# Kernel tuning notes

Hardware: AMD Instinct MI355X
Metric: run time of the kernel (lower is better)

## Reference

```python
import jax, jax.numpy as jnp
import numpy as np

L = 4        # initial_layers (layers actually run in forward)
DIM = 128    # model dim
NB = 8       # num_blocks per layer
K = 2        # max_active blocks per layer
B = 131072   # batch
FIN = 32     # input features (nn.Linear(32, dim))
PRIORITY = 0.5  # fresh block: success_rate*0.6 + excitement*0.4 = 0.5


def setup_inputs() -> dict:
    key = jax.random.key(0)
    ks = jax.random.split(key, 10)
    s = 0.02
    return {
        "x": jax.random.normal(ks[0], (B, FIN), dtype=jnp.float32),
        "proj_w": jax.random.normal(ks[1], (FIN, DIM)) * s,
        "proj_b": jnp.zeros((DIM,)),
        "pos": jax.random.normal(ks[2], (1, 16, DIM)) * 0.02,
        "sel_w": jax.random.normal(ks[3], (L, DIM, NB)) * s,   # per-layer selector
        "sel_b": jnp.zeros((L, NB)),
        "ln_s": jnp.ones((L, NB, DIM)),                         # per-block LayerNorm
        "ln_b": jnp.zeros((L, NB, DIM)),
        "w1": jax.random.normal(ks[4], (L, NB, DIM, 2 * DIM)) * s,
        "b1": jnp.zeros((L, NB, 2 * DIM)),
        "w2": jax.random.normal(ks[5], (L, NB, 2 * DIM, DIM)) * s,
        "b2": jnp.zeros((L, NB, DIM)),
        "gate": jax.random.normal(ks[6], (L, NB, DIM)) * 0.01,  # torsion_gate
        "cls_w": jax.random.normal(ks[7], (DIM, 2)) * s,
        "cls_b": jnp.zeros((2,)),
        "torsion_field": jnp.zeros((1, DIM)),                   # registered buffer (zeros)
    }


def _block(h, ln_s, ln_b, w1, b1, w2, b2, gate, tf):
    # h: [B, 1, DIM]. LayerNorm(eps=1e-5) -> Linear -> GELU -> Linear -> torsion gate -> 0.5 residual
    mu = h.mean(axis=-1, keepdims=True)
    var = ((h - mu) ** 2).mean(axis=-1, keepdims=True)
    hn = (h - mu) / jnp.sqrt(var + 1e-5) * ln_s + ln_b
    z = jax.nn.gelu(hn @ w1 + b1, approximate=False) @ w2 + b2
    te = jax.nn.sigmoid(gate) * tf           # [1, DIM]
    z = z * (1.0 + te[:, None, :])           # broadcast over seq dim (unsqueeze(1))
    return h + 0.5 * z


def reference(x, proj_w, proj_b, pos, sel_w, sel_b, ln_s, ln_b,
              w1, b1, w2, b2, gate, cls_w, cls_b, torsion_field):
    # input projection + positional slice; seq_len == 1
    h = (x @ proj_w + proj_b)[:, None, :] + pos[:, :1, :]   # [B, 1, DIM]
    for l in range(L):
        scores = jax.nn.sigmoid(h.mean(axis=1) @ sel_w[l] + sel_b[l])  # [B, NB]
        # adjusted[0, i] = scores[0, i]*0.6 + priority*0.4 ; top-k taken on row 0
        adj = scores[0] * 0.6 + PRIORITY * 0.4
        _, top = jax.lax.top_k(adj, K)
        for k in range(K):
            i = top[k]
            h = _block(h, ln_s[l][i], ln_b[l][i], w1[l][i], b1[l][i],
                       w2[l][i], b2[l][i], gate[l][i], torsion_field)
    logits = h.mean(axis=1) @ cls_w + cls_b   # [B, 2]
    return logits, h
```

## Files before the change

### kernel.cpp

```cpp
#include <hip/hip_runtime.h>


typedef __attribute__((ext_vector_type(8))) short s16x8;
typedef __attribute__((ext_vector_type(4))) float f32x4;
typedef unsigned short ushort_t;

#define BATCH 131072
#define TBROWS 64
#define HSTR 132
#define FGSTR 544
#define FQSTR 136

#define WS_IDX 0
#define WS_PRM 64
#define WS_PB  12352
#define WS_PW  12864
#define WS_W1  21056
#define WS_W2  545344
#define WS_DMP 1069632

__device__ inline ushort_t f2bf(float f) {
  unsigned u = __float_as_uint(f);
  u += 0x7fffu + ((u >> 16) & 1u);
  return (ushort_t)(u >> 16);
}
__device__ inline ushort_t f2bf1(float f) {
  return (ushort_t)((__float_as_uint(f) + 0x8000u) >> 16);
}
__device__ inline unsigned f2bf2(float lo, float hi) {
  unsigned a = __float_as_uint(lo) + 0x8000u;
  unsigned b = __float_as_uint(hi) + 0x8000u;
  return __builtin_amdgcn_perm(b, a, 0x07060302u);
}

__device__ inline float geluf(float v) {
  float e = __builtin_amdgcn_exp2f(-2.4554670f * v);
  return v * __builtin_amdgcn_rcpf(1.0f + e);
}

__global__ __launch_bounds__(256) void uv6_warm(
    const float* __restrict__ w1, const float* __restrict__ w2,
    float* __restrict__ dump) {
  int gid = blockIdx.x * 256 + threadIdx.x;
  const float4* a = (const float4*)w1;
  const float4* b = (const float4*)w2;
  float s = 0.0f;
#pragma unroll
  for (int i = 0; i < 2; ++i) {
    float4 v = a[gid + i * 131072];
    float4 u = b[gid + i * 131072];
    s += v.x + v.y + v.z + v.w + u.x + u.y + u.z + u.w;
  }
  if (s > 1e30f) dump[0] = s;
}

__global__ __launch_bounds__(1024) void uv6_select(
    const float* __restrict__ x, const float* __restrict__ proj_w,
    const float* __restrict__ proj_b, const float* __restrict__ pos,
    const float* __restrict__ sel_w, const float* __restrict__ sel_b,
    const float* __restrict__ ln_s, const float* __restrict__ ln_b,
    const float* __restrict__ w1, const float* __restrict__ b1,
    const float* __restrict__ w2, const float* __restrict__ b2,
    const float* __restrict__ gate, const float* __restrict__ tf,
    int* __restrict__ wsI) {
  __shared__ float h0[128], hn[128], z1[256];
  __shared__ float red[1024];
  __shared__ float wred[128];
  __shared__ float adjs[8];
  __shared__ int top[2];
  __shared__ float stat[2];
  const int t = threadIdx.x;
  const int lane = t & 63, wv = t >> 6;
  const int n1 = t & 255, dp1 = t >> 8;
  const int n2 = t & 127, dp2 = t >> 7;

  if (t < 128) {
    float a = proj_b[t] + pos[t];
#pragma unroll
    for (int f = 0; f < 32; ++f) a += x[f] * proj_w[f * 128 + t];
    h0[t] = a;
  }
  __syncthreads();

  for (int l = 0; l < 4; ++l) {
    {
      float pp = h0[t >> 3] * sel_w[(l * 128 + (t >> 3)) * 8 + (t & 7)];
      pp += __shfl_xor(pp, 8);
      pp += __shfl_xor(pp, 16);
      pp += __shfl_xor(pp, 32);
      if (lane < 8) wred[wv * 8 + lane] = pp;
    }
    __syncthreads();
    if (t < 8) {
      float sc = sel_b[l * 8 + t];
#pragma unroll
      for (int v = 0; v < 16; ++v) sc += wred[v * 8 + t];
      sc = 1.0f / (1.0f + __expf(-sc));
      adjs[t] = sc * 0.6f + 0.2f;
    }
    __syncthreads();
    if (t == 0) {
      int i0 = 0; float v0 = adjs[0];
      for (int j = 1; j < 8; ++j) if (adjs[j] > v0) { v0 = adjs[j]; i0 = j; }
      int i1 = -1; float v1 = -1e30f;
      for (int j = 0; j < 8; ++j) if (j != i0 && adjs[j] > v1) { v1 = adjs[j]; i1 = j; }
      top[0] = i0; top[1] = i1;
      wsI[2 * l] = i0; wsI[2 * l + 1] = i1;
    }
    __syncthreads();
    for (int kk = 0; kk < 2; ++kk) {
      const int base = l * 8 + top[kk];
      float w1v[32], w2v[32];
      const float* w1p = w1 + (base * 128 + dp1 * 32) * 256 + n1;
      const float* w2p = w2 + (base * 256 + dp2 * 32) * 128 + n2;
#pragma unroll
      for (int j = 0; j < 32; ++j) w1v[j] = w1p[j * 256];
#pragma unroll
      for (int j = 0; j < 32; ++j) w2v[j] = w2p[j * 128];
      if (t < 64) {
        float a = h0[t], b = h0[t + 64];
        float s2 = a + b, q2 = a * a + b * b;
        s2 += __shfl_xor(s2, 1);  q2 += __shfl_xor(q2, 1);
        s2 += __shfl_xor(s2, 2);  q2 += __shfl_xor(q2, 2);
        s2 += __shfl_xor(s2, 4);  q2 += __shfl_xor(q2, 4);
        s2 += __shfl_xor(s2, 8);  q2 += __shfl_xor(q2, 8);
        s2 += __shfl_xor(s2, 16); q2 += __shfl_xor(q2, 16);
        s2 += __shfl_xor(s2, 32); q2 += __shfl_xor(q2, 32);
        if (t == 0) {
          float mu = s2 * (1.0f / 128.0f);
          stat[0] = mu;
          stat[1] = rsqrtf(q2 * (1.0f / 128.0f) - mu * mu + 1e-5f);
        }
      }
      __syncthreads();
      if (t < 128)
        hn[t] = (h0[t] - stat[0]) * stat[1] * ln_s[base * 128 + t] + ln_b[base * 128 + t];
      __syncthreads();
      {
        float a = 0.0f;
#pragma unroll
        for (int j = 0; j < 32; ++j) a += hn[dp1 * 32 + j] * w1v[j];
        red[dp1 * 256 + n1] = a;
      }
      __syncthreads();
      if (t < 256) {
        float z = red[t] + red[256 + t] + red[512 + t] + red[768 + t] + b1[base * 256 + t];
        z1[t] = z * 0.5f * (1.0f + erff(z * 0.70710678118f));
      }
      __syncthreads();
      {
        float a = 0.0f;
#pragma unroll
        for (int j = 0; j < 32; ++j) a += z1[dp2 * 32 + j] * w2v[j];
        red[dp2 * 128 + n2] = a;
      }
      __syncthreads();
      if (t < 128) {
        float z2 = b2[base * 128 + t];
#pragma unroll
        for (int v = 0; v < 8; ++v) z2 += red[v * 128 + t];
        float te = tf[t] * (1.0f / (1.0f + __expf(-gate[base * 128 + t])));
        h0[t] += 0.5f * z2 * (1.0f + te);
      }
      __syncthreads();
    }
  }
}

__global__ __launch_bounds__(256) void uv6_pack(
    const float* __restrict__ w1, const float* __restrict__ w2,
    const float* __restrict__ ln_s, const float* __restrict__ ln_b,
    const float* __restrict__ b1, const float* __restrict__ b2,
    const float* __restrict__ gate, const float* __restrict__ tf,
    const float* __restrict__ proj_w, const float* __restrict__ proj_b,
    const float* __restrict__ pos, const int* __restrict__ wsI,
    ushort_t* __restrict__ w1P, ushort_t* __restrict__ w2P,
    float* __restrict__ wsP, ushort_t* __restrict__ pwP,
    float* __restrict__ pb) {
  const int bx = blockIdx.x;
  if (bx < 2048) {
    int gid = bx * 256 + threadIdx.x;
    int s = gid >> 16, e = gid & 65535;
    int base = (s >> 1) * 8 + wsI[s];
    if (e < 32768) {
      int j = e & 7, ln = (e >> 3) & 63, ks = (e >> 9) & 3, nt = e >> 11;
      int k = ks * 32 + (ln >> 4) * 8 + j;
      int n = nt * 16 + (ln & 15);
      w1P[s * 32768 + e] = f2bf(w1[(base * 128 + k) * 256 + n] * ln_s[base * 128 + k]);
    } else {
      int e2 = e - 32768;
      int j = e2 & 7, ln = (e2 >> 3) & 63, ks = (e2 >> 9) & 7, nt = e2 >> 12;
      int k = ks * 32 + (ln >> 4) * 8 + j;
      int n = nt * 16 + (ln & 15);
      float te = tf[n] * (1.0f / (1.0f + __expf(-gate[base * 128 + n])));
      w2P[s * 32768 + e2] = f2bf(w2[(base * 256 + k) * 128 + n] * (0.5f * (1.0f + te)));
    }
    return;
  }
  if (bx < 2056) {
    int s = bx - 2048, n = threadIdx.x;
    int base = (s >> 1) * 8 + wsI[s];
    float a = b1[base * 256 + n];
#pragma unroll 16
    for (int k = 0; k < 128; ++k)
      a += ln_b[base * 128 + k] * w1[(base * 128 + k) * 256 + n];
    wsP[s * 384 + n] = a;
    if (n < 128) {
      float te = tf[n] * (1.0f / (1.0f + __expf(-gate[base * 128 + n])));
      wsP[s * 384 + 256 + n] = 0.5f * (1.0f + te) * b2[base * 128 + n];
    }
    return;
  }
  int gid = (bx - 2056) * 256 + threadIdx.x;
  if (gid < 4096) {
    int j = gid & 7, ln = (gid >> 3) & 63, nt = gid >> 9;
    int k = (ln >> 4) * 8 + j, n = nt * 16 + (ln & 15);
    pwP[gid] = f2bf(proj_w[k * 128 + n]);
  } else if (gid < 4224) {
    int d = gid - 4096;
    pb[d] = proj_b[d] + pos[d];
  }
}

__global__ __launch_bounds__(512, 2) void uv6_main(
    const float* __restrict__ x, const float* __restrict__ cls_w,
    const float* __restrict__ cls_b, const float* __restrict__ wsP,
    const float* __restrict__ pb, const ushort_t* __restrict__ pwP,
    const ushort_t* __restrict__ w1P, const ushort_t* __restrict__ w2P,
    float* __restrict__ out) {
  __shared__ float hbuf[TBROWS * HSTR];
  __shared__ ushort_t frag[32 * FGSTR];

  const int tid = threadIdx.x;
  const int w = tid >> 6, lane = tid & 63, q = lane >> 4, m0 = lane & 15;
  const int r = tid >> 3, p = tid & 7;
  const int rt_r = r >> 4, m_r = r & 15;
  const long rowbase = (long)blockIdx.x * TBROWS;

  {
    float4 xv = *(const float4*)(x + (rowbase + r) * 32 + p * 4);
    unsigned u01 = f2bf2(xv.x, xv.y), u23 = f2bf2(xv.z, xv.w);
    ushort_t* dst = &frag[(rt_r * 8) * FGSTR + (p >> 1) * FQSTR + m_r * 8 + (p & 1) * 4];
    *(unsigned*)dst = u01;
    *(unsigned*)(dst + 2) = u23;
  }
  __syncthreads();

  {
    s16x8 bfr = *(const s16x8*)(pwP + (w * 64 + lane) * 8);
    float bv = pb[w * 16 + m0];
    f32x4 acc[4];
#pragma unroll
    for (int rt = 0; rt < 4; ++rt) acc[rt] = (f32x4){bv, bv, bv, bv};
#pragma unroll
    for (int rt = 0; rt < 4; ++rt) {
      s16x8 af = *(const s16x8*)&frag[(rt * 8) * FGSTR + q * FQSTR + m0 * 8];
      acc[rt] = __builtin_amdgcn_mfma_f32_16x16x32_bf16(af, bfr, acc[rt], 0, 0, 0);
    }
    int col = w * 16 + m0;
#pragma unroll
    for (int rt = 0; rt < 4; ++rt)
#pragma unroll
      for (int reg = 0; reg < 4; ++reg)
        hbuf[(rt * 16 + 4 * q + reg) * HSTR + col] = acc[rt][reg];
  }
  __syncthreads();

  float* outH = out + (size_t)BATCH * 2;

  for (int s = 0; s < 8; ++s) {
    const float* c1 = wsP + s * 384;
    const float* c2 = c1 + 256;
    const ushort_t* w1s = w1P + s * 32768;
    const ushort_t* w2s = w2P + s * 32768;

    s16x8 bfr1[2][4];
#pragma unroll
    for (int ni = 0; ni < 2; ++ni)
#pragma unroll
      for (int ks = 0; ks < 4; ++ks)
        bfr1[ni][ks] = *(const s16x8*)(w1s + (((2 * w + ni) * 4 + ks) * 64 + lane) * 8);

    {
      const float* hr = hbuf + r * HSTR + p * 16;
      float hv[16];
      *(float4*)(hv) = *(const float4*)(hr);
      *(float4*)(hv + 4) = *(const float4*)(hr + 4);
      *(float4*)(hv + 8) = *(const float4*)(hr + 8);
      *(float4*)(hv + 12) = *(const float4*)(hr + 12);
      float sum = 0.0f, ssq = 0.0f;
#pragma unroll
      for (int i = 0; i < 16; ++i) { sum += hv[i]; ssq += hv[i] * hv[i]; }
      sum += __shfl_xor(sum, 1); ssq += __shfl_xor(ssq, 1);
      sum += __shfl_xor(sum, 2); ssq += __shfl_xor(ssq, 2);
      sum += __shfl_xor(sum, 4); ssq += __shfl_xor(ssq, 4);
      float mu = sum * (1.0f / 128.0f);
      float rstd = rsqrtf(ssq * (1.0f / 128.0f) - mu * mu + 1e-5f);
      float nmu = -mu * rstd;
#pragma unroll
      for (int g = 0; g < 2; ++g) {
        union { unsigned u[4]; s16x8 v; } tv;
#pragma unroll
        for (int jj = 0; jj < 4; ++jj) {
          float a = fmaf(hv[g * 8 + jj * 2], rstd, nmu);
          float b = fmaf(hv[g * 8 + jj * 2 + 1], rstd, nmu);
          tv.u[jj] = f2bf2(a, b);
        }
        int kb = p >> 1, qq = (2 * p + g) & 3;
        *(s16x8*)&frag[(rt_r * 8 + kb) * FGSTR + qq * FQSTR + m_r * 8] = tv.v;
      }
    }
    __syncthreads();

    f32x4 a1[4][2];
    {
#pragma unroll
      for (int ni = 0; ni < 2; ++ni) {
        float bv = c1[(2 * w + ni) * 16 + m0];
#pragma unroll
        for (int rt = 0; rt < 4; ++rt) a1[rt][ni] = (f32x4){bv, bv, bv, bv};
      }
#pragma unroll
      for (int ks = 0; ks < 4; ++ks) {
        s16x8 af[4];
#pragma unroll
        for (int rt = 0; rt < 4; ++rt)
          af[rt] = *(const s16x8*)&frag[(rt * 8 + ks) * FGSTR + q * FQSTR + m0 * 8];
#pragma unroll
        for (int rt = 0; rt < 4; ++rt)
#pragma unroll
          for (int ni = 0; ni < 2; ++ni)
            a1[rt][ni] = __builtin_amdgcn_mfma_f32_16x16x32_bf16(af[rt], bfr1[ni][ks], a1[rt][ni], 0, 0, 0);
      }
    }
    __syncthreads();

    s16x8 bfr2[8];
#pragma unroll
    for (int ks = 0; ks < 8; ++ks)
      bfr2[ks] = *(const s16x8*)(w2s + ((w * 8 + ks) * 64 + lane) * 8);
    f32x4 a2[4];
    {
      float bv = c2[w * 16 + m0];
#pragma unroll
      for (int rt = 0; rt < 4; ++rt) a2[rt] = (f32x4){bv, bv, bv, bv};
    }

    {
      int j = m0 & 7;
#pragma unroll
      for (int ni = 0; ni < 2; ++ni) {
        int qq = (2 * ni + (m0 >> 3)) & 3;
#pragma unroll
        for (int rt = 0; rt < 4; ++rt)
#pragma unroll
          for (int reg = 0; reg < 4; ++reg)
            frag[(rt * 8 + w) * FGSTR + qq * FQSTR + (4 * q + reg) * 8 + j] =
                f2bf1(geluf(a1[rt][ni][reg]));
      }
    }
    __syncthreads();

    {
#pragma unroll
      for (int kb = 0; kb < 8; ++kb) {
        s16x8 af[4];
#pragma unroll
        for (int rt = 0; rt < 4; ++rt)
          af[rt] = *(const s16x8*)&frag[(rt * 8 + kb) * FGSTR + q * FQSTR + m0 * 8];
#pragma unroll
        for (int rt = 0; rt < 4; ++rt)
          a2[rt] = __builtin_amdgcn_mfma_f32_16x16x32_bf16(af[rt], bfr2[kb], a2[rt], 0, 0, 0);
      }
    }

    {
      int col = w * 16 + m0;
#pragma unroll
      for (int rt = 0; rt < 4; ++rt)
#pragma unroll
        for (int reg = 0; reg < 4; ++reg)
          hbuf[(rt * 16 + 4 * q + reg) * HSTR + col] += a2[rt][reg];
    }
    __syncthreads();
  }

#pragma unroll
  for (int it = 0; it < 4; ++it) {
    int p4 = it * 512 + tid;
    int row = p4 >> 5, c = (p4 & 31) * 4;
    float4 o = *(const float4*)(hbuf + row * HSTR + c);
    *(float4*)(outH + rowbase * 128 + p4 * 4) = o;
  }

  {
    const float* hr = hbuf + r * HSTR + p * 16;
    float l0 = 0.0f, l1 = 0.0f;
#pragma unroll
    for (int i = 0; i < 16; i += 4) {
      float4 v = *(const float4*)(hr + i);
      int c = (p * 16 + i) * 2;
      l0 += v.x * cls_w[c] + v.y * cls_w[c + 2] + v.z * cls_w[c + 4] + v.w * cls_w[c + 6];
      l1 += v.x * cls_w[c + 1] + v.y * cls_w[c + 3] + v.z * cls_w[c + 5] + v.w * cls_w[c + 7];
    }
    l0 += __shfl_xor(l0, 1); l1 += __shfl_xor(l1, 1);
    l0 += __shfl_xor(l0, 2); l1 += __shfl_xor(l1, 2);
    l0 += __shfl_xor(l0, 4); l1 += __shfl_xor(l1, 4);
    if (p == 0) {
      float2 lg = {l0 + cls_b[0], l1 + cls_b[1]};
      *(float2*)(out + (rowbase + r) * 2) = lg;
    }
  }
}

extern "C" void kernel_launch(void* const* d_in, const int* in_sizes, int n_in,
                              void* d_out, int out_size, void* d_ws, size_t ws_size,
                              hipStream_t stream) {
  (void)in_sizes; (void)n_in; (void)out_size; (void)ws_size;
  const float* x      = (const float*)d_in[0];
  const float* proj_w = (const float*)d_in[1];
  const float* proj_b = (const float*)d_in[2];
  const float* pos    = (const float*)d_in[3];
  const float* sel_w  = (const float*)d_in[4];
  const float* sel_b  = (const float*)d_in[5];
  const float* ln_s   = (const float*)d_in[6];
  const float* ln_b   = (const float*)d_in[7];
  const float* w1     = (const float*)d_in[8];
  const float* b1     = (const float*)d_in[9];
  const float* w2     = (const float*)d_in[10];
  const float* b2     = (const float*)d_in[11];
  const float* gate   = (const float*)d_in[12];
  const float* cls_w  = (const float*)d_in[13];
  const float* cls_b  = (const float*)d_in[14];
  const float* tf     = (const float*)d_in[15];

  char* ws = (char*)d_ws;
  int* wsI        = (int*)(ws + WS_IDX);
  float* wsP      = (float*)(ws + WS_PRM);
  float* pb       = (float*)(ws + WS_PB);
  ushort_t* pwP   = (ushort_t*)(ws + WS_PW);
  ushort_t* w1P   = (ushort_t*)(ws + WS_W1);
  ushort_t* w2P   = (ushort_t*)(ws + WS_W2);
  float* dump     = (float*)(ws + WS_DMP);
  float* outF     = (float*)d_out;

  uv6_warm<<<512, 256, 0, stream>>>(w1, w2, dump);
  uv6_select<<<1, 1024, 0, stream>>>(x, proj_w, proj_b, pos, sel_w, sel_b, ln_s,
                                     ln_b, w1, b1, w2, b2, gate, tf, wsI);
  uv6_pack<<<2073, 256, 0, stream>>>(w1, w2, ln_s, ln_b, b1, b2, gate, tf,
                                     proj_w, proj_b, pos, wsI, w1P, w2P, wsP,
                                     pwP, pb);
  uv6_main<<<BATCH / TBROWS, 512, 0, stream>>>(x, cls_w, cls_b, wsP, pb, pwP,
                                               w1P, w2P, outF);
}
```

Baseline: 363.3 us.

## Halve main kernel block to 256 threads with doubled per-wave tiles and DPP reductions

The main fused MLP kernel now runs 4 waves per 64-row tile instead of 8. Each wave computes twice as many output columns in every GEMM stage (projection, W1 and W2), and each thread handles 32 columns for LayerNorm and the classifier. The cross-lane reductions switch from shfl_xor to DPP quad permutes. The aim is to reuse each A fragment read from LDS across more MFMAs, cut barrier participants and shuffle cost, at the expense of many more registers per thread (16 W1 fragments, 16 W2 fragments and 16 accumulators), which can cut occupancy or spill.

```diff
diff --git a/kernel.cpp b/kernel.cpp
--- a/kernel.cpp
+++ b/kernel.cpp
@@ -31,6 +31,15 @@
   unsigned a = __float_as_uint(lo) + 0x8000u;
   unsigned b = __float_as_uint(hi) + 0x8000u;
   return __builtin_amdgcn_perm(b, a, 0x07060302u);
+}
+
+__device__ inline float dpp_xor1(float v) {
+  return __int_as_float(__builtin_amdgcn_update_dpp(
+      0, __float_as_int(v), 0xB1 , 0xF, 0xF, true));
+}
+__device__ inline float dpp_xor2(float v) {
+  return __int_as_float(__builtin_amdgcn_update_dpp(
+      0, __float_as_int(v), 0x4E , 0xF, 0xF, true));
 }
 
 __device__ inline float geluf(float v) {
@@ -222,7 +231,7 @@
   }
 }
 
-__global__ __launch_bounds__(512, 2) void uv6_main(
+__global__ __launch_bounds__(256, 2) void uv6_main(
     const float* __restrict__ x, const float* __restrict__ cls_w,
     const float* __restrict__ cls_b, const float* __restrict__ wsP,
     const float* __restrict__ pb, const ushort_t* __restrict__ pwP,
@@ -233,36 +242,46 @@
 
   const int tid = threadIdx.x;
   const int w = tid >> 6, lane = tid & 63, q = lane >> 4, m0 = lane & 15;
-  const int r = tid >> 3, p = tid & 7;
+  const int r = tid >> 2, p = tid & 3;
   const int rt_r = r >> 4, m_r = r & 15;
   const long rowbase = (long)blockIdx.x * TBROWS;
 
   {
-    float4 xv = *(const float4*)(x + (rowbase + r) * 32 + p * 4);
-    unsigned u01 = f2bf2(xv.x, xv.y), u23 = f2bf2(xv.z, xv.w);
-    ushort_t* dst = &frag[(rt_r * 8) * FGSTR + (p >> 1) * FQSTR + m_r * 8 + (p & 1) * 4];
-    *(unsigned*)dst = u01;
-    *(unsigned*)(dst + 2) = u23;
+    const float4* xp = (const float4*)(x + (rowbase + r) * 32 + p * 8);
+    float4 x0 = xp[0], x1 = xp[1];
+    union { unsigned u[4]; s16x8 v; } tv;
+    tv.u[0] = f2bf2(x0.x, x0.y); tv.u[1] = f2bf2(x0.z, x0.w);
+    tv.u[2] = f2bf2(x1.x, x1.y); tv.u[3] = f2bf2(x1.z, x1.w);
+    *(s16x8*)&frag[(rt_r * 8) * FGSTR + p * FQSTR + m_r * 8] = tv.v;
   }
   __syncthreads();
 
   {
-    s16x8 bfr = *(const s16x8*)(pwP + (w * 64 + lane) * 8);
-    float bv = pb[w * 16 + m0];
-    f32x4 acc[4];
-#pragma unroll
-    for (int rt = 0; rt < 4; ++rt) acc[rt] = (f32x4){bv, bv, bv, bv};
+    s16x8 bp0 = *(const s16x8*)(pwP + ((2 * w + 0) * 64 + lane) * 8);
+    s16x8 bp1 = *(const s16x8*)(pwP + ((2 * w + 1) * 64 + lane) * 8);
+    float bv0 = pb[(2 * w + 0) * 16 + m0];
+    float bv1 = pb[(2 * w + 1) * 16 + m0];
+    f32x4 acc[4][2];
+#pragma unroll
+    for (int rt = 0; rt < 4; ++rt) {
+      acc[rt][0] = (f32x4){bv0, bv0, bv0, bv0};
+      acc[rt][1] = (f32x4){bv1, bv1, bv1, bv1};
+    }
 #pragma unroll
     for (int rt = 0; rt < 4; ++rt) {
       s16x8 af = *(const s16x8*)&frag[(rt * 8) * FGSTR + q * FQSTR + m0 * 8];
-      acc[rt] = __builtin_amdgcn_mfma_f32_16x16x32_bf16(af, bfr, acc[rt], 0, 0, 0);
-    }
-    int col = w * 16 + m0;
+      acc[rt][0] = __builtin_amdgcn_mfma_f32_16x16x32_bf16(af, bp0, acc[rt][0], 0, 0, 0);
+      acc[rt][1] = __builtin_amdgcn_mfma_f32_16x16x32_bf16(af, bp1, acc[rt][1], 0, 0, 0);
+    }
 #pragma unroll
     for (int rt = 0; rt < 4; ++rt)
 #pragma unroll
-      for (int reg = 0; reg < 4; ++reg)
-        hbuf[(rt * 16 + 4 * q + reg) * HSTR + col] = acc[rt][reg];
+      for (int ni = 0; ni < 2; ++ni) {
+        int col = (2 * w + ni) * 16 + m0;
+#pragma unroll
+        for (int reg = 0; reg < 4; ++reg)
+          hbuf[(rt * 16 + 4 * q + reg) * HSTR + col] = acc[rt][ni][reg];
+      }
   }
   __syncthreads();
 
@@ -274,138 +293,138 @@
     const ushort_t* w1s = w1P + s * 32768;
     const ushort_t* w2s = w2P + s * 32768;
 
-    s16x8 bfr1[2][4];
-#pragma unroll
-    for (int ni = 0; ni < 2; ++ni)
+    s16x8 bfr1[4][4];
+#pragma unroll
+    for (int ni = 0; ni < 4; ++ni)
 #pragma unroll
       for (int ks = 0; ks < 4; ++ks)
-        bfr1[ni][ks] = *(const s16x8*)(w1s + (((2 * w + ni) * 4 + ks) * 64 + lane) * 8);
+        bfr1[ni][ks] = *(const s16x8*)(w1s + (((4 * w + ni) * 4 + ks) * 64 + lane) * 8);
 
     {
-      const float* hr = hbuf + r * HSTR + p * 16;
-      float hv[16];
-      *(float4*)(hv) = *(const float4*)(hr);
-      *(float4*)(hv + 4) = *(const float4*)(hr + 4);
-      *(float4*)(hv + 8) = *(const float4*)(hr + 8);
-      *(float4*)(hv + 12) = *(const float4*)(hr + 12);
+      const float* hr = hbuf + r * HSTR + p * 32;
+      float hv[32];
+#pragma unroll
+      for (int i = 0; i < 8; ++i)
+        *(float4*)(hv + i * 4) = *(const float4*)(hr + i * 4);
       float sum = 0.0f, ssq = 0.0f;
 #pragma unroll
-      for (int i = 0; i < 16; ++i) { sum += hv[i]; ssq += hv[i] * hv[i]; }
-      sum += __shfl_xor(sum, 1); ssq += __shfl_xor(ssq, 1);
-      sum += __shfl_xor(sum, 2); ssq += __shfl_xor(ssq, 2);
-      sum += __shfl_xor(sum, 4); ssq += __shfl_xor(ssq, 4);
+      for (int i = 0; i < 32; ++i) { sum += hv[i]; ssq += hv[i] * hv[i]; }
+      sum += dpp_xor1(sum); ssq += dpp_xor1(ssq);
+      sum += dpp_xor2(sum); ssq += dpp_xor2(ssq);
       float mu = sum * (1.0f / 128.0f);
       float rstd = rsqrtf(ssq * (1.0f / 128.0f) - mu * mu + 1e-5f);
       float nmu = -mu * rstd;
 #pragma unroll
-      for (int g = 0; g < 2; ++g) {
+      for (int kq = 0; kq < 4; ++kq) {
         union { unsigned u[4]; s16x8 v; } tv;
 #pragma unroll
         for (int jj = 0; jj < 4; ++jj) {
-          float a = fmaf(hv[g * 8 + jj * 2], rstd, nmu);
-          float b = fmaf(hv[g * 8 + jj * 2 + 1], rstd, nmu);
+          float a = fmaf(hv[kq * 8 + jj * 2], rstd, nmu);
+          float b = fmaf(hv[kq * 8 + jj * 2 + 1], rstd, nmu);
           tv.u[jj] = f2bf2(a, b);
         }
-        int kb = p >> 1, qq = (2 * p + g) & 3;
-        *(s16x8*)&frag[(rt_r * 8 + kb) * FGSTR + qq * FQSTR + m_r * 8] = tv.v;
-      }
-    }
-    __syncthreads();
-
-    f32x4 a1[4][2];
-    {
-#pragma unroll
-      for (int ni = 0; ni < 2; ++ni) {
-        float bv = c1[(2 * w + ni) * 16 + m0];
-#pragma unroll
-        for (int rt = 0; rt < 4; ++rt) a1[rt][ni] = (f32x4){bv, bv, bv, bv};
-      }
-#pragma unroll
-      for (int ks = 0; ks < 4; ++ks) {
-        s16x8 af[4];
-#pragma unroll
-        for (int rt = 0; rt < 4; ++rt)
-          af[rt] = *(const s16x8*)&frag[(rt * 8 + ks) * FGSTR + q * FQSTR + m0 * 8];
-#pragma unroll
-        for (int rt = 0; rt < 4; ++rt)
-#pragma unroll
-          for (int ni = 0; ni < 2; ++ni)
-            a1[rt][ni] = __builtin_amdgcn_mfma_f32_16x16x32_bf16(af[rt], bfr1[ni][ks], a1[rt][ni], 0, 0, 0);
-      }
-    }
-    __syncthreads();
-
-    s16x8 bfr2[8];
-#pragma unroll
-    for (int ks = 0; ks < 8; ++ks)
-      bfr2[ks] = *(const s16x8*)(w2s + ((w * 8 + ks) * 64 + lane) * 8);
-    f32x4 a2[4];
-    {
-      float bv = c2[w * 16 + m0];
-#pragma unroll
-      for (int rt = 0; rt < 4; ++rt) a2[rt] = (f32x4){bv, bv, bv, bv};
-    }
+        *(s16x8*)&frag[(rt_r * 8 + p) * FGSTR + kq * FQSTR + m_r * 8] = tv.v;
+      }
+    }
+    __syncthreads();
+
+    f32x4 a1[4][4];
+#pragma unroll
+    for (int ni = 0; ni < 4; ++ni) {
+      float bv = c1[(4 * w + ni) * 16 + m0];
+#pragma unroll
+      for (int rt = 0; rt < 4; ++rt) a1[rt][ni] = (f32x4){bv, bv, bv, bv};
+    }
+#pragma unroll
+    for (int ks = 0; ks < 4; ++ks) {
+      s16x8 af[4];
+#pragma unroll
+      for (int rt = 0; rt < 4; ++rt)
+        af[rt] = *(const s16x8*)&frag[(rt * 8 + ks) * FGSTR + q * FQSTR + m0 * 8];
+#pragma unroll
+      for (int rt = 0; rt < 4; ++rt)
+#pragma unroll
+        for (int ni = 0; ni < 4; ++ni)
+          a1[rt][ni] = __builtin_amdgcn_mfma_f32_16x16x32_bf16(af[rt], bfr1[ni][ks], a1[rt][ni], 0, 0, 0);
+    }
+    __syncthreads();
+
+    s16x8 bfr2[2][8];
+#pragma unroll
+    for (int ni = 0; ni < 2; ++ni)
+#pragma unroll
+      for (int ks = 0; ks < 8; ++ks)
+        bfr2[ni][ks] = *(const s16x8*)(w2s + (((2 * w + ni) * 8 + ks) * 64 + lane) * 8);
+    float cv0 = c2[(2 * w + 0) * 16 + m0];
+    float cv1 = c2[(2 * w + 1) * 16 + m0];
 
     {
       int j = m0 & 7;
 #pragma unroll
+      for (int ni = 0; ni < 4; ++ni) {
+        int kb = 2 * w + (ni >> 1);
+        int kq = (2 * ni + (m0 >> 3)) & 3;
+#pragma unroll
+        for (int rt = 0; rt < 4; ++rt)
+#pragma unroll
+          for (int reg = 0; reg < 4; ++reg)
+            frag[(rt * 8 + kb) * FGSTR + kq * FQSTR + (4 * q + reg) * 8 + j] =
+                f2bf1(geluf(a1[rt][ni][reg]));
+      }
+    }
+    __syncthreads();
+
+    f32x4 a2[4][2];
+#pragma unroll
+    for (int rt = 0; rt < 4; ++rt) {
+      a2[rt][0] = (f32x4){cv0, cv0, cv0, cv0};
+      a2[rt][1] = (f32x4){cv1, cv1, cv1, cv1};
+    }
+#pragma unroll
+    for (int kb = 0; kb < 8; ++kb) {
+      s16x8 af[4];
+#pragma unroll
+      for (int rt = 0; rt < 4; ++rt)
+        af[rt] = *(const s16x8*)&frag[(rt * 8 + kb) * FGSTR + q * FQSTR + m0 * 8];
+#pragma unroll
+      for (int rt = 0; rt < 4; ++rt) {
+        a2[rt][0] = __builtin_amdgcn_mfma_f32_16x16x32_bf16(af[rt], bfr2[0][kb], a2[rt][0], 0, 0, 0);
+        a2[rt][1] = __builtin_amdgcn_mfma_f32_16x16x32_bf16(af[rt], bfr2[1][kb], a2[rt][1], 0, 0, 0);
+      }
+    }
+
+#pragma unroll
+    for (int rt = 0; rt < 4; ++rt)
+#pragma unroll
       for (int ni = 0; ni < 2; ++ni) {
-        int qq = (2 * ni + (m0 >> 3)) & 3;
-#pragma unroll
-        for (int rt = 0; rt < 4; ++rt)
-#pragma unroll
-          for (int reg = 0; reg < 4; ++reg)
-            frag[(rt * 8 + w) * FGSTR + qq * FQSTR + (4 * q + reg) * 8 + j] =
-                f2bf1(geluf(a1[rt][ni][reg]));
-      }
-    }
-    __syncthreads();
-
-    {
-#pragma unroll
-      for (int kb = 0; kb < 8; ++kb) {
-        s16x8 af[4];
-#pragma unroll
-        for (int rt = 0; rt < 4; ++rt)
-          af[rt] = *(const s16x8*)&frag[(rt * 8 + kb) * FGSTR + q * FQSTR + m0 * 8];
-#pragma unroll
-        for (int rt = 0; rt < 4; ++rt)
-          a2[rt] = __builtin_amdgcn_mfma_f32_16x16x32_bf16(af[rt], bfr2[kb], a2[rt], 0, 0, 0);
-      }
-    }
-
-    {
-      int col = w * 16 + m0;
-#pragma unroll
-      for (int rt = 0; rt < 4; ++rt)
+        int col = (2 * w + ni) * 16 + m0;
 #pragma unroll
         for (int reg = 0; reg < 4; ++reg)
-          hbuf[(rt * 16 + 4 * q + reg) * HSTR + col] += a2[rt][reg];
-    }
-    __syncthreads();
-  }
-
-#pragma unroll
-  for (int it = 0; it < 4; ++it) {
-    int p4 = it * 512 + tid;
+          hbuf[(rt * 16 + 4 * q + reg) * HSTR + col] += a2[rt][ni][reg];
+      }
+    __syncthreads();
+  }
+
+#pragma unroll
+  for (int it = 0; it < 8; ++it) {
+    int p4 = it * 256 + tid;
     int row = p4 >> 5, c = (p4 & 31) * 4;
     float4 o = *(const float4*)(hbuf + row * HSTR + c);
     *(float4*)(outH + rowbase * 128 + p4 * 4) = o;
   }
 
   {
-    const float* hr = hbuf + r * HSTR + p * 16;
+    const float* hr = hbuf + r * HSTR + p * 32;
     float l0 = 0.0f, l1 = 0.0f;
 #pragma unroll
-    for (int i = 0; i < 16; i += 4) {
+    for (int i = 0; i < 32; i += 4) {
       float4 v = *(const float4*)(hr + i);
-      int c = (p * 16 + i) * 2;
+      int c = (p * 32 + i) * 2;
       l0 += v.x * cls_w[c] + v.y * cls_w[c + 2] + v.z * cls_w[c + 4] + v.w * cls_w[c + 6];
       l1 += v.x * cls_w[c + 1] + v.y * cls_w[c + 3] + v.z * cls_w[c + 5] + v.w * cls_w[c + 7];
     }
-    l0 += __shfl_xor(l0, 1); l1 += __shfl_xor(l1, 1);
-    l0 += __shfl_xor(l0, 2); l1 += __shfl_xor(l1, 2);
-    l0 += __shfl_xor(l0, 4); l1 += __shfl_xor(l1, 4);
+    l0 += dpp_xor1(l0); l1 += dpp_xor1(l1);
+    l0 += dpp_xor2(l0); l1 += dpp_xor2(l1);
     if (p == 0) {
       float2 lg = {l0 + cls_b[0], l1 + cls_b[1]};
       *(float2*)(out + (rowbase + r) * 2) = lg;
@@ -450,6 +469,6 @@
   uv6_pack<<<2073, 256, 0, stream>>>(w1, w2, ln_s, ln_b, b1, b2, gate, tf,
                                      proj_w, proj_b, pos, wsI, w1P, w2P, wsP,
                                      pwP, pb);
-  uv6_main<<<BATCH / TBROWS, 512, 0, stream>>>(x, cls_w, cls_b, wsP, pb, pwP,
+  uv6_main<<<BATCH / TBROWS, 256, 0, stream>>>(x, cls_w, cls_b, wsP, pb, pwP,
                                                w1P, w2P, outF);
 }
```

After: 371.7 us. 1.02x slower.
